# Kernel optimization log

Measured on AMD Instinct MI355X. Metric: run time of the kernel, lower is better.

The kernel has to match this reference:

```python
import jax, jax.numpy as jnp
import numpy as np

D_MODEL = 512
D_STATE = 64
D_CONV = 4
EXPAND = 2
D_INNER = EXPAND * D_MODEL        # 1024
DT_RANK = D_MODEL // 16           # 32 (official Mamba default)
BATCH, SEQ = 2, 1024


def setup_inputs() -> dict:
    key = jax.random.key(0)
    ks = jax.random.split(key, 16)
    s = 0.02
    rn = lambda k, shape: jax.random.normal(k, shape, jnp.float32) * s
    # A_log init: log(1..d_state) repeated per channel, as in official Mamba
    A_log = jnp.log(jnp.tile(jnp.arange(1, D_STATE + 1, dtype=jnp.float32), (D_INNER, 1)))
    return {
        "x": jax.random.normal(ks[0], (BATCH, SEQ, D_MODEL), jnp.float32),
        # bidirectional wrapper projections
        "W_in_bi": rn(ks[1], (2 * D_MODEL, D_MODEL)),
        "b_in_bi": jnp.zeros((2 * D_MODEL,), jnp.float32),
        "W_out_bi": rn(ks[2], (D_MODEL, D_MODEL)),
        "b_out_bi": jnp.zeros((D_MODEL,), jnp.float32),
        # shared Remamba (Mamba) parameters
        "W_in": rn(ks[3], (2 * D_INNER, D_MODEL)),
        "b_in": jnp.zeros((2 * D_INNER,), jnp.float32),
        "conv_w": rn(ks[4], (D_INNER, 1, D_CONV)),   # depthwise conv kernel
        "conv_b": jnp.zeros((D_INNER,), jnp.float32),
        "W_x": rn(ks[5], (DT_RANK + 2 * D_STATE, D_INNER)),
        "W_dt": rn(ks[6], (D_INNER, DT_RANK)),
        "b_dt": rn(ks[7], (D_INNER,)),
        "A_log": A_log,
        "D_param": jnp.ones((D_INNER,), jnp.float32),
        "W_out": rn(ks[8], (D_MODEL, D_INNER)),
        "b_out": jnp.zeros((D_MODEL,), jnp.float32),
    }


def _mamba(x, W_in, b_in, conv_w, conv_b, W_x, W_dt, b_dt, A_log, D_param, W_out, b_out):
    """Canonical Mamba block. x: (B, L, d_model) -> (B, L, d_model)."""
    B = x.shape[0]
    xz = x @ W_in.T + b_in                       # (B, L, 2*d_inner)
    xin, z = jnp.split(xz, 2, axis=-1)
    # depthwise causal conv over time
    xc = jnp.transpose(xin, (0, 2, 1))            # (B, d_inner, L)
    xc = jnp.pad(xc, ((0, 0), (0, 0), (D_CONV - 1, 0)))
    xc = jax.lax.conv_general_dilated(
        xc, conv_w, (1,), "VALID",
        dimension_numbers=("NCH", "OIH", "NCH"),
        feature_group_count=D_INNER)
    xc = jax.nn.silu(jnp.transpose(xc, (0, 2, 1)) + conv_b)   # (B, L, d_inner)
    # input-dependent dt, B, C
    x_dbl = xc @ W_x.T                            # (B, L, dt_rank + 2*d_state)
    dt, Bm, Cm = jnp.split(x_dbl, [DT_RANK, DT_RANK + D_STATE], axis=-1)
    dt = jax.nn.softplus(dt @ W_dt.T + b_dt)      # (B, L, d_inner)
    A = -jnp.exp(A_log)                           # (d_inner, d_state)

    def step(h, inputs):
        dt_t, B_t, C_t, x_t = inputs              # (B,d_inner),(B,d_state),(B,d_state),(B,d_inner)
        h = jnp.exp(dt_t[..., None] * A) * h + (dt_t * x_t)[..., None] * B_t[:, None, :]
        y = jnp.einsum("bds,bs->bd", h, C_t)
        return h, y

    h0 = jnp.zeros((B, D_INNER, D_STATE), x.dtype)
    xs = (jnp.swapaxes(dt, 0, 1), jnp.swapaxes(Bm, 0, 1),
          jnp.swapaxes(Cm, 0, 1), jnp.swapaxes(xc, 0, 1))
    _, ys = jax.lax.scan(step, h0, xs)            # ys: (L, B, d_inner)
    y = jnp.swapaxes(ys, 0, 1) + xc * D_param
    y = y * jax.nn.silu(z)
    return y @ W_out.T + b_out


def reference(x, W_in_bi, b_in_bi, W_out_bi, b_out_bi,
              W_in, b_in, conv_w, conv_b, W_x, W_dt, b_dt,
              A_log, D_param, W_out, b_out):
    B = x.shape[0]
    xp = x @ W_in_bi.T + b_in_bi                 # (B, L, 2*d_model)
    x_f, x_b = jnp.split(xp, 2, axis=-1)
    # both directions share the same mamba weights -> stack on batch axis
    x_both = jnp.concatenate([x_f, x_b[:, ::-1]], axis=0)
    out = _mamba(x_both, W_in, b_in, conv_w, conv_b, W_x, W_dt, b_dt,
                 A_log, D_param, W_out, b_out)
    out_f, out_b_flip = out[:B], out[B:]
    combined = out_f + out_b_flip[:, ::-1]
    return combined @ W_out_bi.T + b_out_bi
```

## Files before the change

### kernel.cpp

```cpp
#include <hip/hip_runtime.h>
#include <hip/hip_bf16.h>
#include <math.h>

#define SEQL 1024
#define DI 1024
#define DSTATE 64
#define XDBL_N 160
#define MT 4096

typedef short bf16x8 __attribute__((ext_vector_type(8)));
typedef float f32x4 __attribute__((ext_vector_type(4)));

__device__ __forceinline__ unsigned short f2bf(float f) {
    unsigned u = __builtin_bit_cast(unsigned, f);
    u += 0x7FFFu + ((u >> 16) & 1u);
    return (unsigned short)(u >> 16);
}
__device__ __forceinline__ float bf2f(unsigned short h) {
    unsigned u = ((unsigned)h) << 16;
    return __builtin_bit_cast(float, u);
}
__device__ __forceinline__ void gload16(const void* g, void* l) {
    __builtin_amdgcn_global_load_lds((const __attribute__((address_space(1))) void*)g,
                                     (__attribute__((address_space(3))) void*)l, 16, 0, 0);
}
__device__ __forceinline__ float fexp2(float x) {
#if __has_builtin(__builtin_amdgcn_exp2f)
    return __builtin_amdgcn_exp2f(x);
#else
    float r; asm("v_exp_f32 %0, %1" : "=v"(r) : "v"(x)); return r;
#endif
}
__device__ __forceinline__ float dppsum16(float p) {
    int q;
    q = __builtin_amdgcn_update_dpp(0, __builtin_bit_cast(int, p), 0x118, 0xF, 0xF, true);
    p += __builtin_bit_cast(float, q);
    q = __builtin_amdgcn_update_dpp(0, __builtin_bit_cast(int, p), 0x114, 0xF, 0xF, true);
    p += __builtin_bit_cast(float, q);
    q = __builtin_amdgcn_update_dpp(0, __builtin_bit_cast(int, p), 0x112, 0xF, 0xF, true);
    p += __builtin_bit_cast(float, q);
    q = __builtin_amdgcn_update_dpp(0, __builtin_bit_cast(int, p), 0x111, 0xF, 0xF, true);
    p += __builtin_bit_cast(float, q);
    return p;
}

__global__ __launch_bounds__(256) void split_kernel(
    const float* __restrict__ src, unsigned short* __restrict__ h,
    unsigned short* __restrict__ l, int n4)
{
    int i = blockIdx.x * 256 + threadIdx.x;
    if (i >= n4) return;
    float4 v = ((const float4*)src)[i];
    unsigned short h0 = f2bf(v.x), h1 = f2bf(v.y), h2 = f2bf(v.z), h3 = f2bf(v.w);
    unsigned short l0 = f2bf(v.x - bf2f(h0)), l1 = f2bf(v.y - bf2f(h1));
    unsigned short l2 = f2bf(v.z - bf2f(h2)), l3 = f2bf(v.w - bf2f(h3));
    ((uint2*)h)[i] = make_uint2((unsigned)h0 | ((unsigned)h1 << 16), (unsigned)h2 | ((unsigned)h3 << 16));
    ((uint2*)l)[i] = make_uint2((unsigned)l0 | ((unsigned)l1 << 16), (unsigned)l2 | ((unsigned)l3 << 16));
}

template<int ACT, bool TRANS>
__global__ __launch_bounds__(256) void pgemm_kernel(
    const unsigned short* __restrict__ Ah, const unsigned short* __restrict__ Al,
    const unsigned short* __restrict__ Wh, const unsigned short* __restrict__ Wl,
    const float* __restrict__ bias, float* __restrict__ C,
    int M, int N, int K, int lda)
{
    __shared__ unsigned short L[2][4][64 * 32];
    const int tid = threadIdx.x;
    const int bm = blockIdx.y * 64, bn = blockIdx.x * 64;
    const int wv = tid >> 6, lane = tid & 63;
    const int wm = (wv & 1) * 32, wn = (wv >> 1) * 32;
    const int fr = lane & 15, fg = lane >> 4;
    const int srow = tid >> 2, scol = (tid & 3) * 8;

    f32x4 acc[2][2];
    #pragma unroll
    for (int i = 0; i < 2; ++i)
        #pragma unroll
        for (int j = 0; j < 2; ++j) acc[i][j] = (f32x4){0.f, 0.f, 0.f, 0.f};

    const int lo = srow * 32 + scol;
    auto stage = [&](int buf, int kt) {
        const int kc = kt * 32 + scol;
        gload16(Ah + (size_t)(bm + srow) * lda + kc, &L[buf][0][lo]);
        gload16(Al + (size_t)(bm + srow) * lda + kc, &L[buf][1][lo]);
        gload16(Wh + (size_t)(bn + srow) * K + kc, &L[buf][2][lo]);
        gload16(Wl + (size_t)(bn + srow) * K + kc, &L[buf][3][lo]);
    };

    const int NT = K / 32;
    stage(0, 0);
    for (int kt = 0;;) {
        __syncthreads();
        if (kt + 1 < NT) stage((kt + 1) & 1, kt + 1);
        const unsigned short* lah = &L[kt & 1][0][0];
        const unsigned short* lal = &L[kt & 1][1][0];
        const unsigned short* lbh = &L[kt & 1][2][0];
        const unsigned short* lbl = &L[kt & 1][3][0];
        bf16x8 fah[2], fal[2], fbh[2], fbl[2];
        #pragma unroll
        for (int i = 0; i < 2; ++i) {
            const int ra = (wm + i * 16 + fr) * 32 + fg * 8;
            const int rb = (wn + i * 16 + fr) * 32 + fg * 8;
            fah[i] = *(const bf16x8*)&lah[ra];
            fal[i] = *(const bf16x8*)&lal[ra];
            fbh[i] = *(const bf16x8*)&lbh[rb];
            fbl[i] = *(const bf16x8*)&lbl[rb];
        }
        #pragma unroll
        for (int i = 0; i < 2; ++i)
            #pragma unroll
            for (int j = 0; j < 2; ++j) {
                acc[i][j] = __builtin_amdgcn_mfma_f32_16x16x32_bf16(fal[i], fbh[j], acc[i][j], 0, 0, 0);
                acc[i][j] = __builtin_amdgcn_mfma_f32_16x16x32_bf16(fah[i], fbl[j], acc[i][j], 0, 0, 0);
                acc[i][j] = __builtin_amdgcn_mfma_f32_16x16x32_bf16(fah[i], fbh[j], acc[i][j], 0, 0, 0);
            }
        ++kt;
        if (kt >= NT) break;
    }

    #pragma unroll
    for (int i = 0; i < 2; ++i) {
        const int gmb = bm + wm + i * 16 + fg * 4;
        #pragma unroll
        for (int j = 0; j < 2; ++j) {
            const int gn = bn + wn + j * 16 + fr;
            const float bv = bias ? bias[gn] : 0.f;
            float4 v4;
            float* vp = &v4.x;
            #pragma unroll
            for (int r = 0; r < 4; ++r) {
                float v = acc[i][j][r] + bv;
                if (ACT == 1) v = (v > 20.f) ? v : log1pf(__expf(v));
                vp[r] = v;
            }
            if (TRANS) {
                *(float4*)&C[(size_t)gn * M + gmb] = v4;
            } else {
                #pragma unroll
                for (int r = 0; r < 4; ++r) C[(size_t)(gmb + r) * N + gn] = vp[r];
            }
        }
    }
}

template<int ACT, bool DUAL, bool GATE, bool ATRANS>
__global__ __launch_bounds__(256) void agemm_kernel(
    const float* __restrict__ A, const float* __restrict__ Z,
    const unsigned short* __restrict__ Wh, const unsigned short* __restrict__ Wl,
    const float* __restrict__ bias, float* __restrict__ C,
    unsigned short* __restrict__ dh, unsigned short* __restrict__ dl,
    int M, int N, int K, int lda)
{
    __shared__ unsigned short LAh[64 * 40];
    __shared__ unsigned short LAl[64 * 40];
    __shared__ unsigned short LBh[64 * 40];
    __shared__ unsigned short LBl[64 * 40];
    const int tid = threadIdx.x;
    const int bm = blockIdx.y * 64, bn = blockIdx.x * 64;
    const int wv = tid >> 6, lane = tid & 63;
    const int wm = (wv & 1) * 32, wn = (wv >> 1) * 32;
    const int fr = lane & 15, fg = lane >> 4;

    const int srow = tid >> 2, sc = (tid & 3) * 8;
    const unsigned short* Whp = Wh + (size_t)(bn + srow) * K + sc;
    const unsigned short* Wlp = Wl + (size_t)(bn + srow) * K + sc;
    const bool wok = (bn + srow) < N;
    const uint4 zu = {0u, 0u, 0u, 0u};

    const int kp = tid >> 4;
    const int mo = (tid & 15) * 4;
    const float* At0 = ATRANS ? (A + (size_t)(2 * kp) * M + bm + mo) : nullptr;
    const float* At1 = ATRANS ? (At0 + M) : nullptr;
    const float* Zt0 = (ATRANS && GATE) ? (Z + (size_t)(2 * kp) * M + bm + mo) : nullptr;
    const float* Zt1 = (ATRANS && GATE) ? (Zt0 + M) : nullptr;
    const int swg = (kp >> 2) ^ (((tid & 15) >> 1) & 3);
    const int swoff = swg * 8 + (kp & 3) * 2;
    const float* Ap = ATRANS ? nullptr : (A + (size_t)(bm + srow) * lda + sc);

    f32x4 acc[2][2];
    #pragma unroll
    for (int i = 0; i < 2; ++i)
        #pragma unroll
        for (int j = 0; j < 2; ++j) acc[i][j] = (f32x4){0.f, 0.f, 0.f, 0.f};

    alignas(16) float pa0[4], pa1[4], pz0[4], pz1[4];
    alignas(16) float pa[8];
    uint4 pbh, pbl;

    auto prefetch = [&](int k0) {
        if (ATRANS) {
            const size_t off = (size_t)k0 * M;
            *(float4*)&pa0[0] = *(const float4*)(At0 + off);
            *(float4*)&pa1[0] = *(const float4*)(At1 + off);
            if (GATE) {
                *(float4*)&pz0[0] = *(const float4*)(Zt0 + off);
                *(float4*)&pz1[0] = *(const float4*)(Zt1 + off);
            }
        } else {
            *(float4*)&pa[0] = *(const float4*)(Ap + k0);
            *(float4*)&pa[4] = *(const float4*)(Ap + k0 + 4);
        }
        if (wok) {
            pbh = *(const uint4*)(Whp + k0);
            pbl = *(const uint4*)(Wlp + k0);
        } else { pbh = zu; pbl = zu; }
    };

    prefetch(0);
    const int NT = K / 32;
    for (int kt = 0;;) {
        __syncthreads();
        if (ATRANS) {
            #pragma unroll
            for (int j = 0; j < 4; ++j) {
                float v0 = pa0[j], v1 = pa1[j];
                if (GATE) {
                    float z0 = pz0[j], z1 = pz1[j];
                    v0 *= z0 / (1.f + __expf(-z0));
                    v1 *= z1 / (1.f + __expf(-z1));
                }
                unsigned short h0 = f2bf(v0), h1 = f2bf(v1);
                unsigned short l0 = f2bf(v0 - bf2f(h0)), l1 = f2bf(v1 - bf2f(h1));
                const int a = (mo + j) * 40 + swoff;
                *(unsigned*)&LAh[a] = (unsigned)h0 | ((unsigned)h1 << 16);
                *(unsigned*)&LAl[a] = (unsigned)l0 | ((unsigned)l1 << 16);
            }
        } else {
            alignas(16) unsigned short hh[8], ll[8];
            #pragma unroll
            for (int i = 0; i < 8; ++i) {
                float v = pa[i];
                unsigned short h = f2bf(v);
                hh[i] = h; ll[i] = f2bf(v - bf2f(h));
            }
            const int wb = srow * 40 + sc;
            *(uint4*)&LAh[wb] = *(uint4*)&hh[0];
            *(uint4*)&LAl[wb] = *(uint4*)&ll[0];
        }
        {
            const int wb = srow * 40 + sc;
            *(uint4*)&LBh[wb] = pbh;
            *(uint4*)&LBl[wb] = pbl;
        }
        __syncthreads();
        if (kt + 1 < NT) prefetch((kt + 1) * 32);
        bf16x8 fah[2], fal[2], fbh[2], fbl[2];
        #pragma unroll
        for (int i = 0; i < 2; ++i) {
            const int mrow = wm + i * 16 + fr;
            const int g = ATRANS ? (fg ^ ((mrow >> 3) & 3)) : fg;
            const int ra = mrow * 40 + g * 8;
            fah[i] = *(const bf16x8*)&LAh[ra];
            fal[i] = *(const bf16x8*)&LAl[ra];
        }
        #pragma unroll
        for (int j = 0; j < 2; ++j) {
            const int rb = (wn + j * 16 + fr) * 40 + fg * 8;
            fbh[j] = *(const bf16x8*)&LBh[rb];
            fbl[j] = *(const bf16x8*)&LBl[rb];
        }
        #pragma unroll
        for (int i = 0; i < 2; ++i)
            #pragma unroll
            for (int j = 0; j < 2; ++j) {
                acc[i][j] = __builtin_amdgcn_mfma_f32_16x16x32_bf16(fal[i], fbh[j], acc[i][j], 0, 0, 0);
                acc[i][j] = __builtin_amdgcn_mfma_f32_16x16x32_bf16(fah[i], fbl[j], acc[i][j], 0, 0, 0);
                acc[i][j] = __builtin_amdgcn_mfma_f32_16x16x32_bf16(fah[i], fbh[j], acc[i][j], 0, 0, 0);
            }
        ++kt;
        if (kt >= NT) break;
    }

    #pragma unroll
    for (int i = 0; i < 2; ++i) {
        const int gmb = bm + wm + i * 16 + fg * 4;
        #pragma unroll
        for (int j = 0; j < 2; ++j) {
            const int gn = bn + wn + j * 16 + fr;
            if (gn >= N) continue;
            const float bv = bias ? bias[gn] : 0.f;
            #pragma unroll
            for (int r = 0; r < 4; ++r) {
                float v = acc[i][j][r] + bv;
                if (ACT == 1) v = (v > 20.f) ? v : log1pf(__expf(v));
                C[(size_t)(gmb + r) * N + gn] = v;
                if (DUAL && gn < 32) {
                    unsigned short h = f2bf(v);
                    dh[(size_t)(gmb + r) * 32 + gn] = h;
                    dl[(size_t)(gmb + r) * 32 + gn] = f2bf(v - bf2f(h));
                }
            }
        }
    }
}

__global__ __launch_bounds__(256) void reorder_split_kernel(
    const float* __restrict__ xp, unsigned short* __restrict__ xh,
    unsigned short* __restrict__ xl)
{
    int idx = blockIdx.x * 256 + threadIdx.x;
    int c4 = idx & 127;
    int t  = (idx >> 7) & 1023;
    int b4 = idx >> 17;
    float4 v;
    if (b4 < 2) v = *(const float4*)&xp[((size_t)(b4 * SEQL + t)) * DI + c4 * 4];
    else        v = *(const float4*)&xp[((size_t)((b4 - 2) * SEQL + (1023 - t))) * DI + 512 + c4 * 4];
    unsigned short h0 = f2bf(v.x), h1 = f2bf(v.y), h2 = f2bf(v.z), h3 = f2bf(v.w);
    unsigned short l0 = f2bf(v.x - bf2f(h0)), l1 = f2bf(v.y - bf2f(h1));
    unsigned short l2 = f2bf(v.z - bf2f(h2)), l3 = f2bf(v.w - bf2f(h3));
    ((uint2*)xh)[idx] = make_uint2((unsigned)h0 | ((unsigned)h1 << 16), (unsigned)h2 | ((unsigned)h3 << 16));
    ((uint2*)xl)[idx] = make_uint2((unsigned)l0 | ((unsigned)l1 << 16), (unsigned)l2 | ((unsigned)l3 << 16));
}

__global__ __launch_bounds__(256) void conv_silu_T_kernel(
    const float* __restrict__ xinT, const float* __restrict__ cw,
    const float* __restrict__ cb, float* __restrict__ xcT)
{
    int idx = blockIdx.x * 256 + threadIdx.x;
    int t4 = idx & 255;
    int b  = (idx >> 8) & 3;
    int d  = idx >> 10;
    const float* row = xinT + (size_t)d * MT + b * 1024 + t4 * 4;
    float4 cur = *(const float4*)row;
    float p1 = 0.f, p2 = 0.f, p3 = 0.f;
    if (t4 > 0) { float4 pv = *(const float4*)(row - 4); p1 = pv.y; p2 = pv.z; p3 = pv.w; }
    float w0 = cw[d * 4 + 0], w1 = cw[d * 4 + 1], w2 = cw[d * 4 + 2], w3 = cw[d * 4 + 3];
    float bv = cb[d];
    float x0 = p1, x1 = p2, x2 = p3, x3 = cur.x, x4 = cur.y, x5 = cur.z, x6 = cur.w;
    float4 o;
    o.x = bv + w0 * x0 + w1 * x1 + w2 * x2 + w3 * x3;
    o.y = bv + w0 * x1 + w1 * x2 + w2 * x3 + w3 * x4;
    o.z = bv + w0 * x2 + w1 * x3 + w2 * x4 + w3 * x5;
    o.w = bv + w0 * x3 + w1 * x4 + w2 * x5 + w3 * x6;
    o.x *= 1.f / (1.f + __expf(-o.x));
    o.y *= 1.f / (1.f + __expf(-o.y));
    o.z *= 1.f / (1.f + __expf(-o.z));
    o.w *= 1.f / (1.f + __expf(-o.w));
    *(float4*)(xcT + (size_t)d * MT + b * 1024 + t4 * 4) = o;
}

__global__ __launch_bounds__(256, 4) void scan_part1(
    const float* __restrict__ dtT, const float* __restrict__ xcT,
    const float* __restrict__ xdbl, const float* __restrict__ A_log,
    float* __restrict__ Sbuf, float* __restrict__ SDbuf)
{
    const int blk = blockIdx.x;
    const int dblock = blk & 63;
    const int bc = blk >> 6;
    const int bb = bc / 3;
    const int c  = bc - bb * 3;
    const int wave = threadIdx.x >> 6;
    const int lane = threadIdx.x & 63;
    const int dd = lane >> 4;
    const int s4 = lane & 15;
    const int d = dblock * 16 + wave * 4 + dd;
    const float LOG2E = 1.4426950408889634f;

    float A2[4], h[4];
    #pragma unroll
    for (int k = 0; k < 4; ++k) {
        A2[k] = -__expf(A_log[d * DSTATE + s4 * 4 + k]) * LOG2E;
        h[k] = 0.f;
    }
    float sumdt = 0.f;
    const int T0 = c * 256;
    const float* dtR = dtT + (size_t)d * MT + bb * 1024 + T0;
    const float* xcR = xcT + (size_t)d * MT + bb * 1024 + T0;
    const float* Bb = xdbl + ((size_t)bb * SEQL + T0) * XDBL_N + 32 + s4 * 4;

    float4 dt0, xc0, B0[4];
    float4 dt1, xc1, B1[4];

#define L1(t0, dt_, xc_, B_)                                           \
    { dt_ = *(const float4*)(dtR + (t0));                              \
      xc_ = *(const float4*)(xcR + (t0));                              \
      _Pragma("unroll")                                                \
      for (int i = 0; i < 4; ++i)                                      \
        B_[i] = *(const float4*)(Bb + (size_t)((t0) + i) * XDBL_N); }

#define S1(dtv, xcv, Bv)                                               \
    { float dtx = (dtv) * (xcv);                                       \
      sumdt += (dtv);                                                  \
      h[0] = fmaf(fexp2((dtv) * A2[0]), h[0], dtx * Bv.x);             \
      h[1] = fmaf(fexp2((dtv) * A2[1]), h[1], dtx * Bv.y);             \
      h[2] = fmaf(fexp2((dtv) * A2[2]), h[2], dtx * Bv.z);             \
      h[3] = fmaf(fexp2((dtv) * A2[3]), h[3], dtx * Bv.w); }

#define C1(dt_, xc_, B_)                                               \
    { S1(dt_.x, xc_.x, B_[0]); S1(dt_.y, xc_.y, B_[1]);                \
      S1(dt_.z, xc_.z, B_[2]); S1(dt_.w, xc_.w, B_[3]); }

    L1(0, dt0, xc0, B0);
    for (int g = 0; g < 64; g += 2) {
        L1((g + 1) * 4, dt1, xc1, B1);
        C1(dt0, xc0, B0);
        if (g + 2 < 64) L1((g + 2) * 4, dt0, xc0, B0);
        C1(dt1, xc1, B1);
    }
#undef L1
#undef S1
#undef C1

    const size_t so = ((size_t)bc * 1024 + d) * 64 + s4 * 4;
    *(float4*)&Sbuf[so] = make_float4(h[0], h[1], h[2], h[3]);
    if (s4 == 0) SDbuf[bc * 1024 + d] = sumdt;
}

__global__ __launch_bounds__(256, 4) void scan_part2(
    const float* dtT, float* yT,
    const float* __restrict__ xdbl,
    const float* __restrict__ xcT,
    const float* __restrict__ A_log,
    const float* __restrict__ Dpar,
    const float* __restrict__ Sbuf,
    const float* __restrict__ SDbuf)
{
    const int blk = blockIdx.x;
    const int dblock = blk & 63;
    const int bc = blk >> 6;
    const int bb = bc >> 2;
    const int c  = bc & 3;
    const int wave = threadIdx.x >> 6;
    const int lane = threadIdx.x & 63;
    const int dd = lane >> 4;
    const int s4 = lane & 15;
    const int d = dblock * 16 + wave * 4 + dd;
    const float LOG2E = 1.4426950408889634f;

    float A2[4], h[4];
    #pragma unroll
    for (int k = 0; k < 4; ++k) {
        A2[k] = -__expf(A_log[d * DSTATE + s4 * 4 + k]) * LOG2E;
        h[k] = 0.f;
    }
    for (int cc = 0; cc < c; ++cc) {
        const int bcc = bb * 3 + cc;
        const size_t so = ((size_t)bcc * 1024 + d) * 64 + s4 * 4;
        float4 S = *(const float4*)&Sbuf[so];
        float sd = SDbuf[bcc * 1024 + d];
        h[0] = fmaf(fexp2(A2[0] * sd), h[0], S.x);
        h[1] = fmaf(fexp2(A2[1] * sd), h[1], S.y);
        h[2] = fmaf(fexp2(A2[2] * sd), h[2], S.z);
        h[3] = fmaf(fexp2(A2[3] * sd), h[3], S.w);
    }

    const float Dv = Dpar[d];
    const int T0 = c * 256;
    const float* dtR = dtT + (size_t)d * MT + bb * 1024 + T0;
    const float* xcR = xcT + (size_t)d * MT + bb * 1024 + T0;
    float* yR = yT + (size_t)d * MT + bb * 1024 + T0;
    const float* Bb = xdbl + ((size_t)bb * SEQL + T0) * XDBL_N + 32 + s4 * 4;

    float4 dt0, xc0, B0[4], C0[4];
    float4 dt1, xc1, B1[4], C1[4];

#define LOADC(t0, dt_, xc_, B_, C_)                                    \
    { dt_ = *(const float4*)(dtR + (t0));                              \
      xc_ = *(const float4*)(xcR + (t0));                              \
      _Pragma("unroll")                                                \
      for (int i = 0; i < 4; ++i) {                                    \
        const float* bp = Bb + (size_t)((t0) + i) * XDBL_N;            \
        B_[i] = *(const float4*)bp;                                    \
        C_[i] = *(const float4*)(bp + 64);                             \
      } }

#define STEP2(dtv, xcv, Bv, Cv, yref)                                  \
    { float dtx = (dtv) * (xcv);                                       \
      h[0] = fmaf(fexp2((dtv) * A2[0]), h[0], dtx * Bv.x);             \
      h[1] = fmaf(fexp2((dtv) * A2[1]), h[1], dtx * Bv.y);             \
      h[2] = fmaf(fexp2((dtv) * A2[2]), h[2], dtx * Bv.z);             \
      h[3] = fmaf(fexp2((dtv) * A2[3]), h[3], dtx * Bv.w);             \
      float p = h[0] * Cv.x + h[1] * Cv.y + h[2] * Cv.z + h[3] * Cv.w; \
      p = dppsum16(p);                                                 \
      yref = p + (xcv) * Dv; }

#define COMPC(t0, dt_, xc_, B_, C_)                                    \
    { float4 y4;                                                       \
      STEP2(dt_.x, xc_.x, B_[0], C_[0], y4.x);                         \
      STEP2(dt_.y, xc_.y, B_[1], C_[1], y4.y);                         \
      STEP2(dt_.z, xc_.z, B_[2], C_[2], y4.z);                         \
      STEP2(dt_.w, xc_.w, B_[3], C_[3], y4.w);                         \
      if (s4 == 0) *(float4*)(yR + (t0)) = y4; }

    LOADC(0, dt0, xc0, B0, C0);
    for (int g = 0; g < 64; g += 2) {
        LOADC((g + 1) * 4, dt1, xc1, B1, C1);
        COMPC(g * 4, dt0, xc0, B0, C0);
        if (g + 2 < 64) LOADC((g + 2) * 4, dt0, xc0, B0, C0);
        COMPC((g + 1) * 4, dt1, xc1, B1, C1);
    }
#undef LOADC
#undef STEP2
#undef COMPC
}

__global__ __launch_bounds__(256) void combine_kernel(
    const float* __restrict__ out5, float* __restrict__ comb)
{
    int idx = blockIdx.x * 256 + threadIdx.x;
    int c = idx & 511;
    int t = (idx >> 9) & 1023;
    int b = idx >> 19;
    float vf = out5[((size_t)(b * SEQL + t)) * 512 + c];
    float vb = out5[((size_t)((2 + b) * SEQL + (1023 - t))) * 512 + c];
    comb[idx] = vf + vb;
}

extern "C" void kernel_launch(void* const* d_in, const int* in_sizes, int n_in,
                              void* d_out, int out_size, void* d_ws, size_t ws_size,
                              hipStream_t stream)
{
    const float* x        = (const float*)d_in[0];
    const float* W_in_bi  = (const float*)d_in[1];
    const float* b_in_bi  = (const float*)d_in[2];
    const float* W_out_bi = (const float*)d_in[3];
    const float* b_out_bi = (const float*)d_in[4];
    const float* W_in     = (const float*)d_in[5];
    const float* b_in     = (const float*)d_in[6];
    const float* conv_w   = (const float*)d_in[7];
    const float* conv_b   = (const float*)d_in[8];
    const float* W_x      = (const float*)d_in[9];
    const float* W_dt     = (const float*)d_in[10];
    const float* b_dt     = (const float*)d_in[11];
    const float* A_log    = (const float*)d_in[12];
    const float* D_param  = (const float*)d_in[13];
    const float* W_out    = (const float*)d_in[14];
    const float* b_out    = (const float*)d_in[15];
    float* outp = (float*)d_out;
    char* ws = (char*)d_ws;
    const size_t MB = (size_t)1 << 20;
    typedef unsigned short us;

    float* zT   = (float*)(ws + 0);
    float* xp   = (float*)(ws + 0);
    us* Wbi_h   = (us*)(ws + 8 * MB);
    us* Wbi_l   = (us*)(ws + 9 * MB);
    us* Wbi2_h  = (us*)(ws + 0);
    us* Wbi2_l  = (us*)(ws + 524288);
    float* xcT  = (float*)(ws + 16 * MB);
    us* xbh     = (us*)(ws + 16 * MB);
    us* xbl     = (us*)(ws + 20 * MB);
    us* Win_h   = (us*)(ws + 24 * MB);
    us* Win_l   = (us*)(ws + 26 * MB);
    float* out5 = (float*)(ws + 16 * MB);
    us* Wout_h  = (us*)(ws + 24 * MB);
    us* Wout_l  = (us*)(ws + 25 * MB);
    float* comb = (float*)(ws + 26 * MB);
    float* xinT = (float*)(ws + 32 * MB);
    float* dtT  = (float*)(ws + 32 * MB);
    float* xdbl = (float*)(ws + 48 * MB);
    const size_t eb = 48 * MB + 2621440;
    us* Wx_h    = (us*)(ws + eb);
    us* Wx_l    = (us*)(ws + eb + 327680);
    us* Wdt_h   = (us*)(ws + eb + 655360);
    us* Wdt_l   = (us*)(ws + eb + 720896);
    us* dtr_h   = (us*)(ws + eb + 786432);
    us* dtr_l   = (us*)(ws + eb + 1048576);
    float* Sbuf = (float*)(ws + eb);
    float* SDb  = (float*)(ws + eb + 3145728);

    dim3 blk(256, 1, 1);

    split_kernel<<<dim3(512), blk, 0, stream>>>(W_in_bi, Wbi_h, Wbi_l, 131072);
    split_kernel<<<dim3(1024), blk, 0, stream>>>(W_in, Win_h, Win_l, 262144);
    split_kernel<<<dim3(160), blk, 0, stream>>>(W_x, Wx_h, Wx_l, 40960);
    split_kernel<<<dim3(32), blk, 0, stream>>>(W_dt, Wdt_h, Wdt_l, 8192);

    agemm_kernel<0, false, false, false><<<dim3(16, 32), blk, 0, stream>>>(
        x, nullptr, Wbi_h, Wbi_l, b_in_bi, xp, nullptr, nullptr, 2048, 1024, 512, 512);
    reorder_split_kernel<<<dim3(2048), blk, 0, stream>>>(xp, xbh, xbl);
    pgemm_kernel<0, true><<<dim3(16, 64), blk, 0, stream>>>(
        xbh, xbl, Win_h, Win_l, b_in, xinT, 4096, 1024, 512, 512);
    pgemm_kernel<0, true><<<dim3(16, 64), blk, 0, stream>>>(
        xbh, xbl, Win_h + 1024 * 512, Win_l + 1024 * 512, b_in + 1024, zT, 4096, 1024, 512, 512);
    conv_silu_T_kernel<<<dim3(4096), blk, 0, stream>>>(xinT, conv_w, conv_b, xcT);
    agemm_kernel<0, true, false, true><<<dim3(3, 64), blk, 0, stream>>>(
        xcT, nullptr, Wx_h, Wx_l, nullptr, xdbl, dtr_h, dtr_l, 4096, 160, 1024, 0);
    pgemm_kernel<1, true><<<dim3(16, 64), blk, 0, stream>>>(
        dtr_h, dtr_l, Wdt_h, Wdt_l, b_dt, dtT, 4096, 1024, 32, 32);
    scan_part1<<<dim3(768), blk, 0, stream>>>(dtT, xcT, xdbl, A_log, Sbuf, SDb);
    scan_part2<<<dim3(1024), blk, 0, stream>>>(dtT, dtT, xdbl, xcT, A_log, D_param, Sbuf, SDb);
    split_kernel<<<dim3(512), blk, 0, stream>>>(W_out, Wout_h, Wout_l, 131072);
    agemm_kernel<0, false, true, true><<<dim3(8, 64), blk, 0, stream>>>(
        dtT, zT, Wout_h, Wout_l, b_out, out5, nullptr, nullptr, 4096, 512, 1024, 0);
    split_kernel<<<dim3(256), blk, 0, stream>>>(W_out_bi, Wbi2_h, Wbi2_l, 65536);
    combine_kernel<<<dim3(4096), blk, 0, stream>>>(out5, comb);
    agemm_kernel<0, false, false, false><<<dim3(8, 32), blk, 0, stream>>>(
        comb, nullptr, Wbi2_h, Wbi2_l, b_out_bi, outp, nullptr, nullptr, 2048, 512, 512, 512);
}
```

Measured before the change: 330.7 us.

## Split selective scan into eight chunks and pack B/C into a compact buffer

The chunked scan grows from four time chunks per sequence to eight, so part1 and part2 each launch twice as many blocks, and the launch-bound occupancy hint is raised to 8. The x_proj GEMM now writes only the B and C columns into a dense 128-wide buffer that sits in the output allocation, so the scan reads a smaller row stride. Chunk-state buffers are split across workspace and output memory to make room for the extra chunks. The aim is more parallelism and less memory traffic in the sequential scan. In exchange, part2 does a longer serial prefix over earlier chunk states, and the output buffer is reused as scratch, which relies on the final GEMM overwriting it afterwards.

```diff
diff --git a/kernel.cpp b/kernel.cpp
--- a/kernel.cpp
+++ b/kernel.cpp
@@ -7,6 +7,7 @@
 #define DSTATE 64
 #define XDBL_N 160
 #define MT 4096
+#define SPLITBC 21
 
 typedef short bf16x8 __attribute__((ext_vector_type(8)));
 typedef float f32x4 __attribute__((ext_vector_type(4)));
@@ -144,7 +145,7 @@
     }
 }
 
-template<int ACT, bool DUAL, bool GATE, bool ATRANS>
+template<int ACT, bool DUAL, bool GATE, bool ATRANS, bool BCPACK>
 __global__ __launch_bounds__(256) void agemm_kernel(
     const float* __restrict__ A, const float* __restrict__ Z,
     const unsigned short* __restrict__ Wh, const unsigned short* __restrict__ Wl,
@@ -284,7 +285,11 @@
             for (int r = 0; r < 4; ++r) {
                 float v = acc[i][j][r] + bv;
                 if (ACT == 1) v = (v > 20.f) ? v : log1pf(__expf(v));
-                C[(size_t)(gmb + r) * N + gn] = v;
+                if (BCPACK) {
+                    if (gn >= 32) C[(size_t)(gmb + r) * 128 + (gn - 32)] = v;
+                } else {
+                    C[(size_t)(gmb + r) * N + gn] = v;
+                }
                 if (DUAL && gn < 32) {
                     unsigned short h = f2bf(v);
                     dh[(size_t)(gmb + r) * 32 + gn] = h;
@@ -340,16 +345,22 @@
     *(float4*)(xcT + (size_t)d * MT + b * 1024 + t4 * 4) = o;
 }
 
-__global__ __launch_bounds__(256, 4) void scan_part1(
+__device__ __forceinline__ float* sbuf_at(float* SA, float* SB, int bc) {
+    return (bc < SPLITBC) ? (SA + (size_t)bc * 65536) : (SB + (size_t)(bc - SPLITBC) * 65536);
+}
+
+template<int NC>
+__global__ __launch_bounds__(256, 8) void scan_part1(
     const float* __restrict__ dtT, const float* __restrict__ xcT,
-    const float* __restrict__ xdbl, const float* __restrict__ A_log,
-    float* __restrict__ Sbuf, float* __restrict__ SDbuf)
-{
+    const float* __restrict__ bc_buf, const float* __restrict__ A_log,
+    float* SbufA, float* SbufB, float* __restrict__ SDbuf)
+{
+    constexpr int TCH = SEQL / NC;
     const int blk = blockIdx.x;
     const int dblock = blk & 63;
     const int bc = blk >> 6;
-    const int bb = bc / 3;
-    const int c  = bc - bb * 3;
+    const int bb = bc / (NC - 1);
+    const int c  = bc - bb * (NC - 1);
     const int wave = threadIdx.x >> 6;
     const int lane = threadIdx.x & 63;
     const int dd = lane >> 4;
@@ -364,10 +375,10 @@
         h[k] = 0.f;
     }
     float sumdt = 0.f;
-    const int T0 = c * 256;
+    const int T0 = c * TCH;
     const float* dtR = dtT + (size_t)d * MT + bb * 1024 + T0;
     const float* xcR = xcT + (size_t)d * MT + bb * 1024 + T0;
-    const float* Bb = xdbl + ((size_t)bb * SEQL + T0) * XDBL_N + 32 + s4 * 4;
+    const float* Bb = bc_buf + ((size_t)bb * SEQL + T0) * 128 + s4 * 4;
 
     float4 dt0, xc0, B0[4];
     float4 dt1, xc1, B1[4];
@@ -377,7 +388,7 @@
       xc_ = *(const float4*)(xcR + (t0));                              \
       _Pragma("unroll")                                                \
       for (int i = 0; i < 4; ++i)                                      \
-        B_[i] = *(const float4*)(Bb + (size_t)((t0) + i) * XDBL_N); }
+        B_[i] = *(const float4*)(Bb + (size_t)((t0) + i) * 128); }
 
 #define S1(dtv, xcv, Bv)                                               \
     { float dtx = (dtv) * (xcv);                                       \
@@ -392,35 +403,37 @@
       S1(dt_.z, xc_.z, B_[2]); S1(dt_.w, xc_.w, B_[3]); }
 
     L1(0, dt0, xc0, B0);
-    for (int g = 0; g < 64; g += 2) {
+    for (int g = 0; g < TCH / 4; g += 2) {
         L1((g + 1) * 4, dt1, xc1, B1);
         C1(dt0, xc0, B0);
-        if (g + 2 < 64) L1((g + 2) * 4, dt0, xc0, B0);
+        if (g + 2 < TCH / 4) L1((g + 2) * 4, dt0, xc0, B0);
         C1(dt1, xc1, B1);
     }
 #undef L1
 #undef S1
 #undef C1
 
-    const size_t so = ((size_t)bc * 1024 + d) * 64 + s4 * 4;
-    *(float4*)&Sbuf[so] = make_float4(h[0], h[1], h[2], h[3]);
+    float* Sb = sbuf_at(SbufA, SbufB, bc) + (size_t)d * 64 + s4 * 4;
+    *(float4*)Sb = make_float4(h[0], h[1], h[2], h[3]);
     if (s4 == 0) SDbuf[bc * 1024 + d] = sumdt;
 }
 
-__global__ __launch_bounds__(256, 4) void scan_part2(
+template<int NC>
+__global__ __launch_bounds__(256, 8) void scan_part2(
     const float* dtT, float* yT,
-    const float* __restrict__ xdbl,
+    const float* __restrict__ bc_buf,
     const float* __restrict__ xcT,
     const float* __restrict__ A_log,
     const float* __restrict__ Dpar,
-    const float* __restrict__ Sbuf,
+    float* SbufA, float* SbufB,
     const float* __restrict__ SDbuf)
 {
+    constexpr int TCH = SEQL / NC;
     const int blk = blockIdx.x;
     const int dblock = blk & 63;
     const int bc = blk >> 6;
-    const int bb = bc >> 2;
-    const int c  = bc & 3;
+    const int bb = bc / NC;
+    const int c  = bc - bb * NC;
     const int wave = threadIdx.x >> 6;
     const int lane = threadIdx.x & 63;
     const int dd = lane >> 4;
@@ -435,9 +448,9 @@
         h[k] = 0.f;
     }
     for (int cc = 0; cc < c; ++cc) {
-        const int bcc = bb * 3 + cc;
-        const size_t so = ((size_t)bcc * 1024 + d) * 64 + s4 * 4;
-        float4 S = *(const float4*)&Sbuf[so];
+        const int bcc = bb * (NC - 1) + cc;
+        const float* Sb = sbuf_at(SbufA, SbufB, bcc) + (size_t)d * 64 + s4 * 4;
+        float4 S = *(const float4*)Sb;
         float sd = SDbuf[bcc * 1024 + d];
         h[0] = fmaf(fexp2(A2[0] * sd), h[0], S.x);
         h[1] = fmaf(fexp2(A2[1] * sd), h[1], S.y);
@@ -446,11 +459,11 @@
     }
 
     const float Dv = Dpar[d];
-    const int T0 = c * 256;
+    const int T0 = c * TCH;
     const float* dtR = dtT + (size_t)d * MT + bb * 1024 + T0;
     const float* xcR = xcT + (size_t)d * MT + bb * 1024 + T0;
     float* yR = yT + (size_t)d * MT + bb * 1024 + T0;
-    const float* Bb = xdbl + ((size_t)bb * SEQL + T0) * XDBL_N + 32 + s4 * 4;
+    const float* Bb = bc_buf + ((size_t)bb * SEQL + T0) * 128 + s4 * 4;
 
     float4 dt0, xc0, B0[4], C0[4];
     float4 dt1, xc1, B1[4], C1[4];
@@ -460,7 +473,7 @@
       xc_ = *(const float4*)(xcR + (t0));                              \
       _Pragma("unroll")                                                \
       for (int i = 0; i < 4; ++i) {                                    \
-        const float* bp = Bb + (size_t)((t0) + i) * XDBL_N;            \
+        const float* bp = Bb + (size_t)((t0) + i) * 128;               \
         B_[i] = *(const float4*)bp;                                    \
         C_[i] = *(const float4*)(bp + 64);                             \
       } }
@@ -484,10 +497,10 @@
       if (s4 == 0) *(float4*)(yR + (t0)) = y4; }
 
     LOADC(0, dt0, xc0, B0, C0);
-    for (int g = 0; g < 64; g += 2) {
+    for (int g = 0; g < TCH / 4; g += 2) {
         LOADC((g + 1) * 4, dt1, xc1, B1, C1);
         COMPC(g * 4, dt0, xc0, B0, C0);
-        if (g + 2 < 64) LOADC((g + 2) * 4, dt0, xc0, B0, C0);
+        if (g + 2 < TCH / 4) LOADC((g + 2) * 4, dt0, xc0, B0, C0);
         COMPC((g + 1) * 4, dt1, xc1, B1, C1);
     }
 #undef LOADC
@@ -549,7 +562,7 @@
     float* comb = (float*)(ws + 26 * MB);
     float* xinT = (float*)(ws + 32 * MB);
     float* dtT  = (float*)(ws + 32 * MB);
-    float* xdbl = (float*)(ws + 48 * MB);
+    float* SbufA = (float*)(ws + 48 * MB);
     const size_t eb = 48 * MB + 2621440;
     us* Wx_h    = (us*)(ws + eb);
     us* Wx_l    = (us*)(ws + eb + 327680);
@@ -557,8 +570,9 @@
     us* Wdt_l   = (us*)(ws + eb + 720896);
     us* dtr_h   = (us*)(ws + eb + 786432);
     us* dtr_l   = (us*)(ws + eb + 1048576);
-    float* Sbuf = (float*)(ws + eb);
-    float* SDb  = (float*)(ws + eb + 3145728);
+    float* xdblBC = (float*)d_out;
+    float* SbufB  = (float*)d_out + 524288;
+    float* SDb    = (float*)d_out + 983040;
 
     dim3 blk(256, 1, 1);
 
@@ -567,7 +581,7 @@
     split_kernel<<<dim3(160), blk, 0, stream>>>(W_x, Wx_h, Wx_l, 40960);
     split_kernel<<<dim3(32), blk, 0, stream>>>(W_dt, Wdt_h, Wdt_l, 8192);
 
-    agemm_kernel<0, false, false, false><<<dim3(16, 32), blk, 0, stream>>>(
+    agemm_kernel<0, false, false, false, false><<<dim3(16, 32), blk, 0, stream>>>(
         x, nullptr, Wbi_h, Wbi_l, b_in_bi, xp, nullptr, nullptr, 2048, 1024, 512, 512);
     reorder_split_kernel<<<dim3(2048), blk, 0, stream>>>(xp, xbh, xbl);
     pgemm_kernel<0, true><<<dim3(16, 64), blk, 0, stream>>>(
@@ -575,17 +589,19 @@
     pgemm_kernel<0, true><<<dim3(16, 64), blk, 0, stream>>>(
         xbh, xbl, Win_h + 1024 * 512, Win_l + 1024 * 512, b_in + 1024, zT, 4096, 1024, 512, 512);
     conv_silu_T_kernel<<<dim3(4096), blk, 0, stream>>>(xinT, conv_w, conv_b, xcT);
-    agemm_kernel<0, true, false, true><<<dim3(3, 64), blk, 0, stream>>>(
-        xcT, nullptr, Wx_h, Wx_l, nullptr, xdbl, dtr_h, dtr_l, 4096, 160, 1024, 0);
+    agemm_kernel<0, true, false, true, true><<<dim3(3, 64), blk, 0, stream>>>(
+        xcT, nullptr, Wx_h, Wx_l, nullptr, xdblBC, dtr_h, dtr_l, 4096, 160, 1024, 0);
     pgemm_kernel<1, true><<<dim3(16, 64), blk, 0, stream>>>(
         dtr_h, dtr_l, Wdt_h, Wdt_l, b_dt, dtT, 4096, 1024, 32, 32);
-    scan_part1<<<dim3(768), blk, 0, stream>>>(dtT, xcT, xdbl, A_log, Sbuf, SDb);
-    scan_part2<<<dim3(1024), blk, 0, stream>>>(dtT, dtT, xdbl, xcT, A_log, D_param, Sbuf, SDb);
+    scan_part1<8><<<dim3(4 * 7 * 64), blk, 0, stream>>>(
+        dtT, xcT, xdblBC, A_log, SbufA, SbufB, SDb);
+    scan_part2<8><<<dim3(4 * 8 * 64), blk, 0, stream>>>(
+        dtT, dtT, xdblBC, xcT, A_log, D_param, SbufA, SbufB, SDb);
     split_kernel<<<dim3(512), blk, 0, stream>>>(W_out, Wout_h, Wout_l, 131072);
-    agemm_kernel<0, false, true, true><<<dim3(8, 64), blk, 0, stream>>>(
+    agemm_kernel<0, false, true, true, false><<<dim3(8, 64), blk, 0, stream>>>(
         dtT, zT, Wout_h, Wout_l, b_out, out5, nullptr, nullptr, 4096, 512, 1024, 0);
     split_kernel<<<dim3(256), blk, 0, stream>>>(W_out_bi, Wbi2_h, Wbi2_l, 65536);
     combine_kernel<<<dim3(4096), blk, 0, stream>>>(out5, comb);
-    agemm_kernel<0, false, false, false><<<dim3(8, 32), blk, 0, stream>>>(
+    agemm_kernel<0, false, false, false, false><<<dim3(8, 32), blk, 0, stream>>>(
         comb, nullptr, Wbi2_h, Wbi2_l, b_out_bi, outp, nullptr, nullptr, 2048, 512, 512, 512);
 }
```

Measured after the change: 1.133 ms. 243% more time.

## Stage scan inputs through double-buffered LDS using async global-to-LDS loads

Applied to the files above, without the earlier changes.

Both scan kernels now copy tiles of 32 timesteps of B/C, dt and xc into shared memory with global_load_lds, double-buffered and synchronized per tile. Each thread previously issued its own global float4 loads for B and C, which were redundant across the 4 d-rows in a block. Sharing the loads in LDS cuts global traffic and instruction count. In exchange the kernels use more LDS and add a block barrier per tile, which may limit occupancy.

```diff
diff --git a/kernel.cpp b/kernel.cpp
--- a/kernel.cpp
+++ b/kernel.cpp
@@ -345,16 +345,21 @@
     const float* __restrict__ xdbl, const float* __restrict__ A_log,
     float* __restrict__ Sbuf, float* __restrict__ SDbuf)
 {
+    __shared__ float BL[2][32 * 64];
+    __shared__ float dtL[2][16 * 32];
+    __shared__ float xcL[2][16 * 32];
     const int blk = blockIdx.x;
     const int dblock = blk & 63;
-    const int bc = blk >> 6;
-    const int bb = bc / 3;
-    const int c  = bc - bb * 3;
-    const int wave = threadIdx.x >> 6;
-    const int lane = threadIdx.x & 63;
+    const int bcn = blk >> 6;
+    const int bb = bcn / 3;
+    const int c  = bcn - bb * 3;
+    const int tid = threadIdx.x;
+    const int wave = tid >> 6;
+    const int lane = tid & 63;
     const int dd = lane >> 4;
     const int s4 = lane & 15;
     const int d = dblock * 16 + wave * 4 + dd;
+    const int dloc = wave * 4 + dd;
     const float LOG2E = 1.4426950408889634f;
 
     float A2[4], h[4];
@@ -365,46 +370,57 @@
     }
     float sumdt = 0.f;
     const int T0 = c * 256;
-    const float* dtR = dtT + (size_t)d * MT + bb * 1024 + T0;
-    const float* xcR = xcT + (size_t)d * MT + bb * 1024 + T0;
-    const float* Bb = xdbl + ((size_t)bb * SEQL + T0) * XDBL_N + 32 + s4 * 4;
-
-    float4 dt0, xc0, B0[4];
-    float4 dt1, xc1, B1[4];
-
-#define L1(t0, dt_, xc_, B_)                                           \
-    { dt_ = *(const float4*)(dtR + (t0));                              \
-      xc_ = *(const float4*)(xcR + (t0));                              \
-      _Pragma("unroll")                                                \
-      for (int i = 0; i < 4; ++i)                                      \
-        B_[i] = *(const float4*)(Bb + (size_t)((t0) + i) * XDBL_N); }
-
-#define S1(dtv, xcv, Bv)                                               \
-    { float dtx = (dtv) * (xcv);                                       \
-      sumdt += (dtv);                                                  \
-      h[0] = fmaf(fexp2((dtv) * A2[0]), h[0], dtx * Bv.x);             \
-      h[1] = fmaf(fexp2((dtv) * A2[1]), h[1], dtx * Bv.y);             \
-      h[2] = fmaf(fexp2((dtv) * A2[2]), h[2], dtx * Bv.z);             \
-      h[3] = fmaf(fexp2((dtv) * A2[3]), h[3], dtx * Bv.w); }
-
-#define C1(dt_, xc_, B_)                                               \
-    { S1(dt_.x, xc_.x, B_[0]); S1(dt_.y, xc_.y, B_[1]);                \
-      S1(dt_.z, xc_.z, B_[2]); S1(dt_.w, xc_.w, B_[3]); }
-
-    L1(0, dt0, xc0, B0);
-    for (int g = 0; g < 64; g += 2) {
-        L1((g + 1) * 4, dt1, xc1, B1);
-        C1(dt0, xc0, B0);
-        if (g + 2 < 64) L1((g + 2) * 4, dt0, xc0, B0);
-        C1(dt1, xc1, B1);
-    }
-#undef L1
-#undef S1
-#undef C1
-
-    const size_t so = ((size_t)bc * 1024 + d) * 64 + s4 * 4;
+    const float* BCb = xdbl + ((size_t)bb * SEQL + T0) * XDBL_N + 32;
+    const float* dtb = dtT + (size_t)(dblock * 16) * MT + bb * 1024 + T0;
+    const float* xcb = xcT + (size_t)(dblock * 16) * MT + bb * 1024 + T0;
+
+    auto stage = [&](int buf, int tile) {
+        const int t0 = tile * 32;
+        #pragma unroll
+        for (int q = 0; q < 2; ++q) {
+            const int idx = q * 256 + tid;
+            gload16(BCb + (size_t)(t0 + (idx >> 4)) * XDBL_N + (idx & 15) * 4,
+                    &BL[buf][idx * 4]);
+        }
+        if (tid < 128) {
+            gload16(dtb + (size_t)(tid >> 3) * MT + t0 + (tid & 7) * 4,
+                    &dtL[buf][tid * 4]);
+        } else {
+            const int idx = tid - 128;
+            gload16(xcb + (size_t)(idx >> 3) * MT + t0 + (idx & 7) * 4,
+                    &xcL[buf][idx * 4]);
+        }
+    };
+
+    stage(0, 0);
+    for (int tile = 0;;) {
+        __syncthreads();
+        if (tile + 1 < 8) stage((tile + 1) & 1, tile + 1);
+        const int buf = tile & 1;
+        #pragma unroll
+        for (int i = 0; i < 32; i += 4) {
+            float4 dt4 = *(const float4*)&dtL[buf][dloc * 32 + i];
+            float4 xc4 = *(const float4*)&xcL[buf][dloc * 32 + i];
+            #pragma unroll
+            for (int j = 0; j < 4; ++j) {
+                float dtv = (&dt4.x)[j];
+                float xcv = (&xc4.x)[j];
+                float4 B = *(const float4*)&BL[buf][(i + j) * 64 + s4 * 4];
+                float dtx = dtv * xcv;
+                sumdt += dtv;
+                h[0] = fmaf(fexp2(dtv * A2[0]), h[0], dtx * B.x);
+                h[1] = fmaf(fexp2(dtv * A2[1]), h[1], dtx * B.y);
+                h[2] = fmaf(fexp2(dtv * A2[2]), h[2], dtx * B.z);
+                h[3] = fmaf(fexp2(dtv * A2[3]), h[3], dtx * B.w);
+            }
+        }
+        ++tile;
+        if (tile == 8) break;
+    }
+
+    const size_t so = ((size_t)bcn * 1024 + d) * 64 + s4 * 4;
     *(float4*)&Sbuf[so] = make_float4(h[0], h[1], h[2], h[3]);
-    if (s4 == 0) SDbuf[bc * 1024 + d] = sumdt;
+    if (s4 == 0) SDbuf[bcn * 1024 + d] = sumdt;
 }
 
 __global__ __launch_bounds__(256, 4) void scan_part2(
@@ -416,16 +432,22 @@
     const float* __restrict__ Sbuf,
     const float* __restrict__ SDbuf)
 {
+    __shared__ float BL[2][32 * 64];
+    __shared__ float CL[2][32 * 64];
+    __shared__ float dtL[2][16 * 32];
+    __shared__ float xcL[2][16 * 32];
     const int blk = blockIdx.x;
     const int dblock = blk & 63;
-    const int bc = blk >> 6;
-    const int bb = bc >> 2;
-    const int c  = bc & 3;
-    const int wave = threadIdx.x >> 6;
-    const int lane = threadIdx.x & 63;
+    const int bcn = blk >> 6;
+    const int bb = bcn >> 2;
+    const int c  = bcn & 3;
+    const int tid = threadIdx.x;
+    const int wave = tid >> 6;
+    const int lane = tid & 63;
     const int dd = lane >> 4;
     const int s4 = lane & 15;
     const int d = dblock * 16 + wave * 4 + dd;
+    const int dloc = wave * 4 + dd;
     const float LOG2E = 1.4426950408889634f;
 
     float A2[4], h[4];
@@ -447,52 +469,66 @@
 
     const float Dv = Dpar[d];
     const int T0 = c * 256;
-    const float* dtR = dtT + (size_t)d * MT + bb * 1024 + T0;
-    const float* xcR = xcT + (size_t)d * MT + bb * 1024 + T0;
+    const float* BCb = xdbl + ((size_t)bb * SEQL + T0) * XDBL_N + 32;
+    const float* dtb = dtT + (size_t)(dblock * 16) * MT + bb * 1024 + T0;
+    const float* xcb = xcT + (size_t)(dblock * 16) * MT + bb * 1024 + T0;
     float* yR = yT + (size_t)d * MT + bb * 1024 + T0;
-    const float* Bb = xdbl + ((size_t)bb * SEQL + T0) * XDBL_N + 32 + s4 * 4;
-
-    float4 dt0, xc0, B0[4], C0[4];
-    float4 dt1, xc1, B1[4], C1[4];
-
-#define LOADC(t0, dt_, xc_, B_, C_)                                    \
-    { dt_ = *(const float4*)(dtR + (t0));                              \
-      xc_ = *(const float4*)(xcR + (t0));                              \
-      _Pragma("unroll")                                                \
-      for (int i = 0; i < 4; ++i) {                                    \
-        const float* bp = Bb + (size_t)((t0) + i) * XDBL_N;            \
-        B_[i] = *(const float4*)bp;                                    \
-        C_[i] = *(const float4*)(bp + 64);                             \
-      } }
-
-#define STEP2(dtv, xcv, Bv, Cv, yref)                                  \
-    { float dtx = (dtv) * (xcv);                                       \
-      h[0] = fmaf(fexp2((dtv) * A2[0]), h[0], dtx * Bv.x);             \
-      h[1] = fmaf(fexp2((dtv) * A2[1]), h[1], dtx * Bv.y);             \
-      h[2] = fmaf(fexp2((dtv) * A2[2]), h[2], dtx * Bv.z);             \
-      h[3] = fmaf(fexp2((dtv) * A2[3]), h[3], dtx * Bv.w);             \
-      float p = h[0] * Cv.x + h[1] * Cv.y + h[2] * Cv.z + h[3] * Cv.w; \
-      p = dppsum16(p);                                                 \
-      yref = p + (xcv) * Dv; }
-
-#define COMPC(t0, dt_, xc_, B_, C_)                                    \
-    { float4 y4;                                                       \
-      STEP2(dt_.x, xc_.x, B_[0], C_[0], y4.x);                         \
-      STEP2(dt_.y, xc_.y, B_[1], C_[1], y4.y);                         \
-      STEP2(dt_.z, xc_.z, B_[2], C_[2], y4.z);                         \
-      STEP2(dt_.w, xc_.w, B_[3], C_[3], y4.w);                         \
-      if (s4 == 0) *(float4*)(yR + (t0)) = y4; }
-
-    LOADC(0, dt0, xc0, B0, C0);
-    for (int g = 0; g < 64; g += 2) {
-        LOADC((g + 1) * 4, dt1, xc1, B1, C1);
-        COMPC(g * 4, dt0, xc0, B0, C0);
-        if (g + 2 < 64) LOADC((g + 2) * 4, dt0, xc0, B0, C0);
-        COMPC((g + 1) * 4, dt1, xc1, B1, C1);
-    }
-#undef LOADC
-#undef STEP2
-#undef COMPC
+
+    auto stage = [&](int buf, int tile) {
+        const int t0 = tile * 32;
+        #pragma unroll
+        for (int q = 0; q < 2; ++q) {
+            const int idx = q * 256 + tid;
+            gload16(BCb + (size_t)(t0 + (idx >> 4)) * XDBL_N + (idx & 15) * 4,
+                    &BL[buf][idx * 4]);
+        }
+        #pragma unroll
+        for (int q = 0; q < 2; ++q) {
+            const int idx = q * 256 + tid;
+            gload16(BCb + (size_t)(t0 + (idx >> 4)) * XDBL_N + 64 + (idx & 15) * 4,
+                    &CL[buf][idx * 4]);
+        }
+        if (tid < 128) {
+            gload16(dtb + (size_t)(tid >> 3) * MT + t0 + (tid & 7) * 4,
+                    &dtL[buf][tid * 4]);
+        } else {
+            const int idx = tid - 128;
+            gload16(xcb + (size_t)(idx >> 3) * MT + t0 + (idx & 7) * 4,
+                    &xcL[buf][idx * 4]);
+        }
+    };
+
+    stage(0, 0);
+    for (int tile = 0;;) {
+        __syncthreads();
+        if (tile + 1 < 8) stage((tile + 1) & 1, tile + 1);
+        const int buf = tile & 1;
+        const int tg = tile * 32;
+        #pragma unroll
+        for (int i = 0; i < 32; i += 4) {
+            float4 dt4 = *(const float4*)&dtL[buf][dloc * 32 + i];
+            float4 xc4 = *(const float4*)&xcL[buf][dloc * 32 + i];
+            float4 y4;
+            #pragma unroll
+            for (int j = 0; j < 4; ++j) {
+                float dtv = (&dt4.x)[j];
+                float xcv = (&xc4.x)[j];
+                float4 B = *(const float4*)&BL[buf][(i + j) * 64 + s4 * 4];
+                float4 C = *(const float4*)&CL[buf][(i + j) * 64 + s4 * 4];
+                float dtx = dtv * xcv;
+                h[0] = fmaf(fexp2(dtv * A2[0]), h[0], dtx * B.x);
+                h[1] = fmaf(fexp2(dtv * A2[1]), h[1], dtx * B.y);
+                h[2] = fmaf(fexp2(dtv * A2[2]), h[2], dtx * B.z);
+                h[3] = fmaf(fexp2(dtv * A2[3]), h[3], dtx * B.w);
+                float p = h[0] * C.x + h[1] * C.y + h[2] * C.z + h[3] * C.w;
+                p = dppsum16(p);
+                (&y4.x)[j] = p + xcv * Dv;
+            }
+            if (s4 == 0) *(float4*)(yR + tg + i) = y4;
+        }
+        ++tile;
+        if (tile == 8) break;
+    }
 }
 
 __global__ __launch_bounds__(256) void combine_kernel(
```

New measurement: 305.6 us. 7.6% less time.
